# Kernel optimization log

Measured on AMD Instinct MI355X. Metric: run time of the kernel, lower is better.

The kernel has to match this reference:

```python
import jax, jax.numpy as jnp
import numpy as np

EPS = 1e-7  # keras backend epsilon
S = 64.0
M = 0.5
B, D, NC = 1024, 512, 50000


def setup_inputs() -> dict:
    key = jax.random.key(0)
    kx, kw, kl = jax.random.split(key, 3)
    x = jax.random.normal(kx, (B, D), dtype=jnp.float32)
    W = jax.random.normal(kw, (D, NC), dtype=jnp.float32)
    labels = jax.random.randint(kl, (B,), 0, NC)
    y = jax.nn.one_hot(labels, NC, dtype=jnp.float32)  # [B, NC] one-hot targets
    return {"x": x, "y": y, "W": W}


def reference(x, y, W):
    # L2-normalize embeddings (rows) and class weights (columns)
    xn = x / jnp.linalg.norm(x, axis=1, keepdims=True)
    Wn = W / jnp.linalg.norm(W, axis=0, keepdims=True)
    logits = xn @ Wn  # [B, NC] cosine similarities
    theta = jnp.arccos(jnp.clip(logits, -1.0 + EPS, 1.0 - EPS))
    target_logits = jnp.cos(theta + M)
    logits = logits * (1.0 - y) + target_logits * y
    logits = logits * S
    return jax.nn.softmax(logits, axis=-1)
```

## Files before the change

### kernel.cpp

```cpp
#include <hip/hip_runtime.h>
#include <hip/hip_fp16.h>
#include <cstdint>
#include <cstddef>

#define NCLS 50000
#define DIM 512
#define NROW 1024
#define NTN 391

typedef _Float16 half8 __attribute__((ext_vector_type(8)));
typedef float f32x4 __attribute__((ext_vector_type(4)));

#define AS1(p) ((const __attribute__((address_space(1))) void*)(p))
#define AS3(p) ((__attribute__((address_space(3))) void*)(p))

__global__ void prep_x_kernel(const float* __restrict__ x,
                              __half* __restrict__ xh,
                              float* __restrict__ rn)
{
    int row = blockIdx.x;
    int l = threadIdx.x;
    const float4* xr = (const float4*)(x + (size_t)row * DIM);
    __half2* dst = (__half2*)(xh + (size_t)row * DIM);
    float s = 0.f;
#pragma unroll
    for (int i = 0; i < 2; ++i) {
        int idx = l + i * 64;
        float4 v = xr[idx];
        dst[idx * 2]     = __floats2half2_rn(v.x, v.y);
        dst[idx * 2 + 1] = __floats2half2_rn(v.z, v.w);
        s += v.x * v.x + v.y * v.y + v.z * v.z + v.w * v.w;
    }
#pragma unroll
    for (int off = 32; off > 0; off >>= 1) s += __shfl_down(s, off);
    if (l == 0) rn[row] = rsqrtf(s);
}

__global__ void transpose_w_kernel(const float* __restrict__ W,
                                   __half* __restrict__ Wt,
                                   float* __restrict__ part)
{
    __shared__ float tile[64][65];
    __shared__ float cpart[4][64];
    int n0 = blockIdx.x * 64;
    int k0 = blockIdx.y * 64;
    int t = threadIdx.x;
    int f4 = t & 15;
    int kr = t >> 4;
    int n = n0 + f4 * 4;
    bool ok = (n < NCLS);
#pragma unroll
    for (int i = 0; i < 4; ++i) {
        int k = kr + i * 16;
        float4 v = ok ? *(const float4*)(W + (size_t)(k0 + k) * NCLS + n)
                      : make_float4(0.f, 0.f, 0.f, 0.f);
        tile[k][f4 * 4 + 0] = v.x;
        tile[k][f4 * 4 + 1] = v.y;
        tile[k][f4 * 4 + 2] = v.z;
        tile[k][f4 * 4 + 3] = v.w;
    }
    __syncthreads();
#pragma unroll
    for (int i = 0; i < 8; ++i) {
        int idx = t + i * 256;
        int nn = idx >> 5;
        int kp = idx & 31;
        int gn = n0 + nn;
        if (gn < NCLS) {
            __half2 h = __floats2half2_rn(tile[kp * 2][nn], tile[kp * 2 + 1][nn]);
            *(__half2*)(Wt + (size_t)gn * DIM + k0 + kp * 2) = h;
        }
    }
    {
        int nn = t & 63;
        int seg = t >> 6;
        float s = 0.f;
#pragma unroll
        for (int k = 0; k < 16; ++k) {
            float v = tile[seg * 16 + k][nn];
            s += v * v;
        }
        cpart[seg][nn] = s;
        __syncthreads();
        if (t < 64 && n0 + t < NCLS) {
            part[(size_t)blockIdx.y * NCLS + n0 + t] =
                cpart[0][t] + cpart[1][t] + cpart[2][t] + cpart[3][t];
        }
    }
}

__global__ void make_cn_kernel(const float* __restrict__ part, float* __restrict__ cn)
{
    int c = blockIdx.x * 256 + threadIdx.x;
    if (c >= NCLS) return;
    float s = 0.f;
#pragma unroll
    for (int j = 0; j < 8; ++j) s += part[(size_t)j * NCLS + c];
    cn[c] = rsqrtf(s);
}

__global__ void find_labels_kernel(const float4* __restrict__ y4, int* __restrict__ lab)
{
    int i4 = blockIdx.x * 256 + threadIdx.x;
    float4 v = y4[i4];
    if (v.x != 0.f || v.y != 0.f || v.z != 0.f || v.w != 0.f) {
        long base = (long)i4 * 4;
        if (v.x != 0.f) { long i = base + 0; lab[i / NCLS] = (int)(i % NCLS); }
        if (v.y != 0.f) { long i = base + 1; lab[i / NCLS] = (int)(i % NCLS); }
        if (v.z != 0.f) { long i = base + 2; lab[i / NCLS] = (int)(i % NCLS); }
        if (v.w != 0.f) { long i = base + 3; lab[i / NCLS] = (int)(i % NCLS); }
    }
}

template<int PASS>
__global__ __launch_bounds__(256, 4) void gemm_arc_kernel(
    const __half* __restrict__ A,
    const __half* __restrict__ Bt,
    const float* __restrict__ rn,
    const float* __restrict__ cn,
    const int* __restrict__ lab,
    const float* __restrict__ rs,
    float* __restrict__ out,
    float* __restrict__ rowpart)
{
    __shared__ __align__(16) __half As[128 * 64];
    __shared__ __align__(16) __half Bs[128 * 64];
    __shared__ float rsum[2][128];

    const int tid = threadIdx.x;
    const int wid = tid >> 6;
    const int lane = tid & 63;
    const int wm = wid >> 1;
    const int wn = wid & 1;

    const int b = blockIdx.x;
    const int w = (b & 7) * NTN + (b >> 3);
    const int mt = w & 7;
    const int nt = w >> 3;
    const int tileM = mt * 128;
    const int tileN = nt * 128;

    const int srow = lane >> 3;
    const int sblk = (lane & 7) ^ srow;

    f32x4 acc[4][4] = {};

    auto stage = [&](int k0) {
#pragma unroll
        for (int c = 0; c < 4; ++c) {
            int chunk = wid * 4 + c;
            int row = chunk * 8 + srow;
            const __half* sa = A + (size_t)(tileM + row) * DIM + k0 + sblk * 8;
            __builtin_amdgcn_global_load_lds(AS1(sa), AS3((char*)As + chunk * 1024), 16, 0, 0);
            int gn = tileN + row;
            if (gn > NCLS - 1) gn = NCLS - 1;
            const __half* sb = Bt + (size_t)gn * DIM + k0 + sblk * 8;
            __builtin_amdgcn_global_load_lds(AS1(sb), AS3((char*)Bs + chunk * 1024), 16, 0, 0);
        }
    };

    auto compute = [&]() {
        const int krow = lane >> 4;
        const int rl = lane & 15;
#pragma unroll
        for (int kk = 0; kk < 2; ++kk) {
            half8 af[4], bf[4];
#pragma unroll
            for (int m = 0; m < 4; ++m) {
                int r = wm * 64 + m * 16 + rl;
                int kb = (kk * 4 + krow) ^ (r & 7);
                af[m] = *(const half8*)((const char*)As + r * 128 + kb * 16);
            }
#pragma unroll
            for (int n = 0; n < 4; ++n) {
                int r = wn * 64 + n * 16 + rl;
                int kb = (kk * 4 + krow) ^ (r & 7);
                bf[n] = *(const half8*)((const char*)Bs + r * 128 + kb * 16);
            }
#pragma unroll
            for (int m = 0; m < 4; ++m)
#pragma unroll
                for (int n = 0; n < 4; ++n)
                    acc[m][n] = __builtin_amdgcn_mfma_f32_16x16x32_f16(af[m], bf[n], acc[m][n], 0, 0, 0);
        }
    };

#pragma unroll 1
    for (int k0 = 0; k0 < DIM; k0 += 64) {
        stage(k0);
        __syncthreads();
        compute();
        __syncthreads();
    }

    const float cosM = 0.8775825618903728f;
    const float sinM = 0.4794255386042030f;
    const int col_l = lane & 15;
    const int rgrp = lane >> 4;
    float* buf = (float*)As;

#pragma unroll
    for (int m = 0; m < 4; ++m) {
        int lr0 = wm * 64 + m * 16 + rgrp * 4;
        int gr0 = tileM + lr0;
        float rnv[4]; int labv[4]; float rsv[4];
#pragma unroll
        for (int r = 0; r < 4; ++r) {
            rnv[r] = rn[gr0 + r];
            labv[r] = lab[gr0 + r];
            if (PASS == 1) rsv[r] = rs[gr0 + r];
        }
        float rowacc[4] = {0.f, 0.f, 0.f, 0.f};
#pragma unroll
        for (int n = 0; n < 4; ++n) {
            int gc = tileN + wn * 64 + n * 16 + col_l;
            bool okc = (gc < NCLS);
            float cnv = okc ? cn[gc] : 0.f;
#pragma unroll
            for (int r = 0; r < 4; ++r) {
                float cv = acc[m][n][r] * rnv[r] * cnv;
                float logit;
                if (gc == labv[r]) {
                    float cc = fminf(fmaxf(cv, -1.f + 1e-7f), 1.f - 1e-7f);
                    logit = 64.f * (cc * cosM - sqrtf(1.f - cc * cc) * sinM);
                } else {
                    logit = 64.f * cv;
                }
                float e = __expf(logit);
                if (PASS == 0) {
                    if (okc) rowacc[r] += e;
                } else {
                    buf[(wm * 16 + rgrp * 4 + r) * 128 + wn * 64 + n * 16 + col_l] = e * rsv[r];
                }
            }
        }
        if (PASS == 0) {
#pragma unroll
            for (int r = 0; r < 4; ++r) {
                float s = rowacc[r];
                s += __shfl_xor(s, 1);
                s += __shfl_xor(s, 2);
                s += __shfl_xor(s, 4);
                s += __shfl_xor(s, 8);
                if (col_l == 0) rsum[wn][lr0 + r] = s;
            }
        } else {
            __syncthreads();
#pragma unroll
            for (int i = 0; i < 4; ++i) {
                int idx = tid + i * 256;
                int lr = idx >> 5;
                int c4 = idx & 31;
                int gr = tileM + (lr >> 4) * 64 + m * 16 + (lr & 15);
                int gcl = tileN + c4 * 4;
                if (gcl < NCLS)
                    *(float4*)(out + (size_t)gr * NCLS + gcl) = ((float4*)buf)[idx];
            }
            __syncthreads();
        }
    }
    if (PASS == 0) {
        __syncthreads();
        if (tid < 128) {
            float tot = rsum[0][tid] + rsum[1][tid];
            rowpart[(size_t)nt * NROW + tileM + tid] = tot;
        }
    }
}

__global__ void reduce_rs_kernel(const float* __restrict__ rowpart, float* __restrict__ rs)
{
    int row = blockIdx.x * 256 + threadIdx.x;
    float s = 0.f;
    for (int t = 0; t < NTN; ++t) s += rowpart[(size_t)t * NROW + row];
    rs[row] = 1.f / s;
}

extern "C" void kernel_launch(void* const* d_in, const int* in_sizes, int n_in,
                              void* d_out, int out_size, void* d_ws, size_t ws_size,
                              hipStream_t stream)
{
    const float* x = (const float*)d_in[0];
    const float* y = (const float*)d_in[1];
    const float* W = (const float*)d_in[2];
    float* out = (float*)d_out;

    char* ws = (char*)d_ws;
    __half* Wt     = (__half*)(ws);
    __half* xh     = (__half*)(ws + 51200000);
    float* rn      = (float*) (ws + 52248576);
    float* cn      = (float*) (ws + 52252672);
    float* part    = (float*) (ws + 52452672);
    float* rowpart = part;
    int*   lab     = (int*)   (ws + 54054208);
    float* rs      = (float*) (ws + 54058304);

    hipLaunchKernelGGL(prep_x_kernel, dim3(NROW), dim3(64), 0, stream, x, xh, rn);
    hipLaunchKernelGGL(transpose_w_kernel, dim3(782, 8), dim3(256), 0, stream, W, Wt, part);
    hipLaunchKernelGGL(make_cn_kernel, dim3(196), dim3(256), 0, stream, part, cn);
    hipLaunchKernelGGL(find_labels_kernel, dim3(50000), dim3(256), 0, stream, (const float4*)y, lab);
    hipLaunchKernelGGL(gemm_arc_kernel<0>, dim3(8 * NTN), dim3(256), 0, stream,
                       xh, Wt, rn, cn, lab, rs, out, rowpart);
    hipLaunchKernelGGL(reduce_rs_kernel, dim3(4), dim3(256), 0, stream, rowpart, rs);
    hipLaunchKernelGGL(gemm_arc_kernel<1>, dim3(8 * NTN), dim3(256), 0, stream,
                       xh, Wt, rn, cn, lab, rs, out, rowpart);
}
```

Baseline: 255.0 us.

## Enlarge GEMM tile to 256x128 with 512-thread blocks and XCD-aware remap

Switches the fused GEMM+ArcFace kernel from 128x128 tiles run by 256 threads to 256x128 tiles run by 512 threads (8 waves), so each staged W tile is reused across twice as many rows. This halves how often W is re-read from global memory in both passes. The block-index remap is rewritten to hand out contiguous work ranges per XCD for the new grid of 1564 blocks. It doubles LDS use per block and adds threads, which may cut the number of resident blocks per CU.

New measurement: 266.3 us. 1.04x slower.

```diff
diff --git a/kernel.cpp b/kernel.cpp
--- a/kernel.cpp
+++ b/kernel.cpp
@@ -7,6 +7,7 @@
 #define DIM 512
 #define NROW 1024
 #define NTN 391
+#define NWG 1564
 
 typedef _Float16 half8 __attribute__((ext_vector_type(8)));
 typedef float f32x4 __attribute__((ext_vector_type(4)));
@@ -113,7 +114,7 @@
 }
 
 template<int PASS>
-__global__ __launch_bounds__(256, 4) void gemm_arc_kernel(
+__global__ __launch_bounds__(512, 4) void gemm_arc_kernel(
     const __half* __restrict__ A,
     const __half* __restrict__ Bt,
     const float* __restrict__ rn,
@@ -123,59 +124,62 @@
     float* __restrict__ out,
     float* __restrict__ rowpart)
 {
-    __shared__ __align__(16) __half As[128 * 64];
+    __shared__ __align__(16) __half As[256 * 64];
     __shared__ __align__(16) __half Bs[128 * 64];
-    __shared__ float rsum[2][128];
+    __shared__ float rsum[2][256];
 
     const int tid = threadIdx.x;
     const int wid = tid >> 6;
     const int lane = tid & 63;
     const int wm = wid >> 1;
     const int wn = wid & 1;
-
-    const int b = blockIdx.x;
-    const int w = (b & 7) * NTN + (b >> 3);
-    const int mt = w & 7;
-    const int nt = w >> 3;
-    const int tileM = mt * 128;
+    const int rl = lane & 15;
+    const int krow = lane >> 4;
+
+    const int orig = blockIdx.x;
+    const int xcd = orig & 7;
+    const int q = NWG >> 3, r8 = NWG & 7;
+    const int base_w = (xcd < r8) ? xcd * (q + 1) : r8 * (q + 1) + (xcd - r8) * q;
+    const int w = base_w + (orig >> 3);
+    const int mt = w & 3;
+    const int nt = w >> 2;
+    const int tileM = mt * 256;
     const int tileN = nt * 128;
 
-    const int srow = lane >> 3;
-    const int sblk = (lane & 7) ^ srow;
-
     f32x4 acc[4][4] = {};
 
+    const int srr = tid >> 3;
+    const int sblk = (tid & 7) ^ (srr & 7);
     auto stage = [&](int k0) {
 #pragma unroll
         for (int c = 0; c < 4; ++c) {
-            int chunk = wid * 4 + c;
-            int row = chunk * 8 + srow;
-            const __half* sa = A + (size_t)(tileM + row) * DIM + k0 + sblk * 8;
-            __builtin_amdgcn_global_load_lds(AS1(sa), AS3((char*)As + chunk * 1024), 16, 0, 0);
-            int gn = tileN + row;
+            const __half* sa = A + (size_t)(tileM + c * 64 + srr) * DIM + k0 + sblk * 8;
+            __builtin_amdgcn_global_load_lds(AS1(sa), AS3((char*)As + c * 8192 + tid * 16), 16, 0, 0);
+        }
+#pragma unroll
+        for (int c = 0; c < 2; ++c) {
+            int gn = tileN + c * 64 + srr;
             if (gn > NCLS - 1) gn = NCLS - 1;
             const __half* sb = Bt + (size_t)gn * DIM + k0 + sblk * 8;
-            __builtin_amdgcn_global_load_lds(AS1(sb), AS3((char*)Bs + chunk * 1024), 16, 0, 0);
+            __builtin_amdgcn_global_load_lds(AS1(sb), AS3((char*)Bs + c * 8192 + tid * 16), 16, 0, 0);
         }
     };
 
     auto compute = [&]() {
-        const int krow = lane >> 4;
-        const int rl = lane & 15;
 #pragma unroll
         for (int kk = 0; kk < 2; ++kk) {
             half8 af[4], bf[4];
 #pragma unroll
             for (int m = 0; m < 4; ++m) {
-                int r = wm * 64 + m * 16 + rl;
-                int kb = (kk * 4 + krow) ^ (r & 7);
-                af[m] = *(const half8*)((const char*)As + r * 128 + kb * 16);
+                int row = wm * 64 + m * 16 + rl;
+                int kb = (kk * 4 + krow) ^ (row & 7);
+                af[m] = *(const half8*)((const char*)As + row * 128 + kb * 16);
             }
 #pragma unroll
             for (int n = 0; n < 4; ++n) {
-                int r = wn * 64 + n * 16 + rl;
-                int kb = (kk * 4 + krow) ^ (r & 7);
-                bf[n] = *(const half8*)((const char*)Bs + r * 128 + kb * 16);
+                int row = wn * 64 + n * 16 + rl;
+                int kb = (kk * 4 + krow) ^ (row & 7);
+                bf[n] = *(const half8*)((const char*)Bs + row * 128 + kb * 16);
             }
 #pragma unroll
             for (int m = 0; m < 4; ++m)
@@ -195,8 +199,8 @@
 
     const float cosM = 0.8775825618903728f;
     const float sinM = 0.4794255386042030f;
-    const int col_l = lane & 15;
-    const int rgrp = lane >> 4;
+    const int col_l = rl;
+    const int rgrp = krow;
     float* buf = (float*)As;
 
 #pragma unroll
@@ -248,7 +252,7 @@
             __syncthreads();
 #pragma unroll
             for (int i = 0; i < 4; ++i) {
-                int idx = tid + i * 256;
+                int idx = tid + i * 512;
                 int lr = idx >> 5;
                 int c4 = idx & 31;
                 int gr = tileM + (lr >> 4) * 64 + m * 16 + (lr & 15);
@@ -261,7 +265,7 @@
     }
     if (PASS == 0) {
         __syncthreads();
-        if (tid < 128) {
+        if (tid < 256) {
             float tot = rsum[0][tid] + rsum[1][tid];
             rowpart[(size_t)nt * NROW + tileM + tid] = tot;
         }
@@ -299,9 +303,9 @@
     hipLaunchKernelGGL(transpose_w_kernel, dim3(782, 8), dim3(256), 0, stream, W, Wt, part);
     hipLaunchKernelGGL(make_cn_kernel, dim3(196), dim3(256), 0, stream, part, cn);
     hipLaunchKernelGGL(find_labels_kernel, dim3(50000), dim3(256), 0, stream, (const float4*)y, lab);
-    hipLaunchKernelGGL(gemm_arc_kernel<0>, dim3(8 * NTN), dim3(256), 0, stream,
+    hipLaunchKernelGGL(gemm_arc_kernel<0>, dim3(NWG), dim3(512), 0, stream,
                        xh, Wt, rn, cn, lab, rs, out, rowpart);
     hipLaunchKernelGGL(reduce_rs_kernel, dim3(4), dim3(256), 0, stream, rowpart, rs);
-    hipLaunchKernelGGL(gemm_arc_kernel<1>, dim3(8 * NTN), dim3(256), 0, stream,
+    hipLaunchKernelGGL(gemm_arc_kernel<1>, dim3(NWG), dim3(512), 0, stream,
                        xh, Wt, rn, cn, lab, rs, out, rowpart);
 }
```

## Double-buffer GEMM K-loop with async LDS prefetch of the next K slice

Applied to the files above, without the earlier changes.

Replaces the single-buffered 64-wide K step (load, sync, compute, sync) with a two-slot LDS ring of 32-wide K slices. The next slice is prefetched with global_load_lds while the current one feeds the MFMAs, gated by explicit vmcnt waits and raw barriers. It also raises wave priority around the MFMA block and uses a new 4-way XOR swizzle. This targets load latency left exposed by the synchronous loop, at the cost of twice as many barrier rounds and fragile hand-written waitcnt ordering.

After: 265.9 us. 1.04x slower.

```diff
diff --git a/kernel.cpp b/kernel.cpp
--- a/kernel.cpp
+++ b/kernel.cpp
@@ -123,8 +123,7 @@
     float* __restrict__ out,
     float* __restrict__ rowpart)
 {
-    __shared__ __align__(16) __half As[128 * 64];
-    __shared__ __align__(16) __half Bs[128 * 64];
+    __shared__ __align__(16) char ring[2][16384];
     __shared__ float rsum[2][128];
 
     const int tid = threadIdx.x;
@@ -132,6 +131,9 @@
     const int lane = tid & 63;
     const int wm = wid >> 1;
     const int wn = wid & 1;
+    const int rl = lane & 15;
+    const int krow = lane >> 4;
+    const int koff = (krow ^ (rl & 3)) * 16;
 
     const int b = blockIdx.x;
     const int w = (b & 7) * NTN + (b >> 3);
@@ -140,64 +142,66 @@
     const int tileM = mt * 128;
     const int tileN = nt * 128;
 
-    const int srow = lane >> 3;
-    const int sblk = (lane & 7) ^ srow;
-
     f32x4 acc[4][4] = {};
 
-    auto stage = [&](int k0) {
-#pragma unroll
-        for (int c = 0; c < 4; ++c) {
-            int chunk = wid * 4 + c;
-            int row = chunk * 8 + srow;
-            const __half* sa = A + (size_t)(tileM + row) * DIM + k0 + sblk * 8;
-            __builtin_amdgcn_global_load_lds(AS1(sa), AS3((char*)As + chunk * 1024), 16, 0, 0);
-            int gn = tileN + row;
-            if (gn > NCLS - 1) gn = NCLS - 1;
-            const __half* sb = Bt + (size_t)gn * DIM + k0 + sblk * 8;
-            __builtin_amdgcn_global_load_lds(AS1(sb), AS3((char*)Bs + chunk * 1024), 16, 0, 0);
-        }
+    const int row0 = tid >> 2;
+    const int row1 = row0 + 64;
+    const int p0 = (tid & 3) ^ (row0 & 3);
+    const int p1 = (tid & 3) ^ (row1 & 3);
+    const __half* aS0 = A + (size_t)(tileM + row0) * DIM + p0 * 8;
+    const __half* aS1 = A + (size_t)(tileM + row1) * DIM + p1 * 8;
+    int gn0 = tileN + row0; if (gn0 > NCLS - 1) gn0 = NCLS - 1;
+    int gn1 = tileN + row1; if (gn1 > NCLS - 1) gn1 = NCLS - 1;
+    const __half* bS0 = Bt + (size_t)gn0 * DIM + p0 * 8;
+    const __half* bS1 = Bt + (size_t)gn1 * DIM + p1 * 8;
+    const int ldsBase = wid * 1024;
+
+    auto stage = [&](int h) {
+        char* s = ring[h & 1];
+        const int ko = h * 32;
+        __builtin_amdgcn_global_load_lds(AS1(aS0 + ko), AS3(s + ldsBase), 16, 0, 0);
+        __builtin_amdgcn_global_load_lds(AS1(aS1 + ko), AS3(s + 4096 + ldsBase), 16, 0, 0);
+        __builtin_amdgcn_global_load_lds(AS1(bS0 + ko), AS3(s + 8192 + ldsBase), 16, 0, 0);
+        __builtin_amdgcn_global_load_lds(AS1(bS1 + ko), AS3(s + 12288 + ldsBase), 16, 0, 0);
     };
 
-    auto compute = [&]() {
-        const int krow = lane >> 4;
-        const int rl = lane & 15;
-#pragma unroll
-        for (int kk = 0; kk < 2; ++kk) {
-            half8 af[4], bf[4];
-#pragma unroll
-            for (int m = 0; m < 4; ++m) {
-                int r = wm * 64 + m * 16 + rl;
-                int kb = (kk * 4 + krow) ^ (r & 7);
-                af[m] = *(const half8*)((const char*)As + r * 128 + kb * 16);
-            }
-#pragma unroll
-            for (int n = 0; n < 4; ++n) {
-                int r = wn * 64 + n * 16 + rl;
-                int kb = (kk * 4 + krow) ^ (r & 7);
-                bf[n] = *(const half8*)((const char*)Bs + r * 128 + kb * 16);
-            }
-#pragma unroll
-            for (int m = 0; m < 4; ++m)
-#pragma unroll
-                for (int n = 0; n < 4; ++n)
-                    acc[m][n] = __builtin_amdgcn_mfma_f32_16x16x32_f16(af[m], bf[n], acc[m][n], 0, 0, 0);
-        }
-    };
+    stage(0);
 
 #pragma unroll 1
-    for (int k0 = 0; k0 < DIM; k0 += 64) {
-        stage(k0);
-        __syncthreads();
-        compute();
-        __syncthreads();
-    }
+    for (int h = 0; h < 16; ++h) {
+        __builtin_amdgcn_s_barrier();
+        if (h < 15) {
+            stage(h + 1);
+            asm volatile("s_waitcnt vmcnt(4)" ::: "memory");
+        } else {
+            asm volatile("s_waitcnt vmcnt(0)" ::: "memory");
+        }
+        __builtin_amdgcn_s_barrier();
+        __builtin_amdgcn_sched_barrier(0);
+
+        const char* s = ring[h & 1];
+        half8 af[4], bf[4];
+#pragma unroll
+        for (int m = 0; m < 4; ++m)
+            af[m] = *(const half8*)(s + (wm * 64 + m * 16 + rl) * 64 + koff);
+#pragma unroll
+        for (int n = 0; n < 4; ++n)
+            bf[n] = *(const half8*)(s + 8192 + (wn * 64 + n * 16 + rl) * 64 + koff);
+        __builtin_amdgcn_s_setprio(1);
+#pragma unroll
+        for (int m = 0; m < 4; ++m)
+#pragma unroll
+            for (int n = 0; n < 4; ++n)
+                acc[m][n] = __builtin_amdgcn_mfma_f32_16x16x32_f16(af[m], bf[n], acc[m][n], 0, 0, 0);
+        __builtin_amdgcn_s_setprio(0);
+    }
+    __syncthreads();
 
     const float cosM = 0.8775825618903728f;
     const float sinM = 0.4794255386042030f;
-    const int col_l = lane & 15;
-    const int rgrp = lane >> 4;
-    float* buf = (float*)As;
+    const int col_l = rl;
+    const int rgrp = krow;
+    float* buf = (float*)ring;
 
 #pragma unroll
     for (int m = 0; m < 4; ++m) {
```
